# Optimization experiments

Measured on AMD Instinct MI355X. Metric: run time of the kernel, lower is better.

Reference implementation:

```python
import jax, jax.numpy as jnp
import numpy as np

BINS = 10


def _neg_pearson(p, t):
    # global standardization (torch.std default is unbiased, ddof=1)
    p = (p - p.mean()) / p.std(ddof=1)
    t = (t - t.mean()) / t.std(ddof=1)
    N = p.shape[1]
    sx = p.sum(1); sy = t.sum(1)
    sxy = (p * t).sum(1)
    sx2 = (p * p).sum(1); sy2 = (t * t).sum(1)
    pear = (N * sxy - sx * sy) / jnp.sqrt((N * sx2 - sx**2) * (N * sy2 - sy**2))
    return (1.0 - pear).mean()


def _hann(N):
    # torch.hann_window is periodic: 0.5*(1 - cos(2*pi*n/N))
    return 0.5 * (1.0 - jnp.cos(2.0 * jnp.pi * jnp.arange(N, dtype=jnp.float32) / N))


def _phase_correlation(x, t):
    # torch.stft with n_fft=seq_len, center=False, hann window -> single frame = rfft(x*hann)
    N = x.shape[1]
    w = _hann(N)
    xf = jnp.fft.rfft(x * w, axis=1)   # [B, N//2+1]
    tf = jnp.fft.rfft(t * w, axis=1)
    corr = xf * jnp.conj(tf)
    corr = corr / jnp.abs(corr)        # phase-only correlation
    cm = jnp.fft.irfft(corr, n=N, axis=1)  # [B, N]
    idx = jnp.argmax(cm, axis=1)
    return 1.0 - jnp.mean(jnp.cos(2.0 * jnp.pi * idx / N))


def _power_spectrum(x, t):
    xp = jnp.abs(jnp.fft.rfft(x, axis=1)) ** 2
    tp = jnp.abs(jnp.fft.rfft(t, axis=1)) ** 2
    return jnp.mean(jnp.abs(xp - tp)) / jnp.mean(tp)


def _mutual_information(x, y, bins=BINS):
    B, S = x.shape
    xmin = x.min(1); xmax = x.max(1)
    ymin = y.min(1); ymax = y.max(1)
    bwx = (xmax - xmin) / bins
    bwy = (ymax - ymin) / bins
    ix = jnp.clip(((x - xmin[:, None]) / bwx[:, None]).astype(jnp.int32), 0, bins - 1)
    iy = jnp.clip(((y - ymin[:, None]) / bwy[:, None]).astype(jnp.int32), 0, bins - 1)
    flat = ix * bins + iy  # [B, S]
    # vectorized 2D histogram via scatter-add (replaces the python double loop)
    hist = jax.vmap(lambda f: jnp.zeros(bins * bins, jnp.float32).at[f].add(1.0))(flat)
    hist = hist.reshape(B, bins, bins)
    hx = hist.sum(2); hy = hist.sum(1)
    denom = B * S  # NOTE: original normalizes by batch*seq (faithful reproduction)
    px = hx / denom; py = hy / denom; pxy = hist / denom
    eps = 1e-8
    mi = (pxy * jnp.log((pxy + eps) / (px[:, :, None] * py[:, None, :] + eps))).sum((1, 2))
    hxe = -(px * jnp.log(px + eps)).sum(1)
    hye = -(py * jnp.log(py + eps)).sum(1)
    nmi = mi / ((hxe + hye) / 2.0)
    return 1.0 - nmi.mean()


def setup_inputs() -> dict:
    key = jax.random.key(0)
    k1, k2 = jax.random.split(key)
    return {
        "predictions": jax.random.normal(k1, (2, 512, 16384), dtype=jnp.float32),
        "targets": jax.random.normal(k2, (512, 16384), dtype=jnp.float32),
        "i": 0,
        "epoch": 700,
    }


def reference(predictions, targets, i, epoch):
    p = predictions[i]  # [B, S]
    loss = _neg_pearson(p, targets)
    if epoch >= 400:
        loss = loss + _phase_correlation(p, targets)
        loss = loss + _power_spectrum(p, targets)
    if epoch >= 700:
        loss = loss + _mutual_information(p, targets)
    return loss
```

## Files before the change

kernel.cpp:

```cpp
#include <hip/hip_runtime.h>
#include <math.h>

#define BB 512
#define SS 16384
#define TPIF 6.28318530717958647692f

#define PD(i) ((i) + ((i) >> 4) + ((i) >> 8))
#define NPD 17472

__device__ __forceinline__ int sp(int k) {
    int s = ((k & 7) << 11) + (((k >> 3) & 7) << 8) + (((k >> 6) & 7) << 5)
          + (((k >> 9) & 7) << 2) + ((k >> 12) & 3);
    return PD(s);
}


template <int SGN, int LOG2Q>
__device__ __forceinline__ void stage_dif8(float2* sz, int t) {
    constexpr int Q = 1 << LOG2Q;
    constexpr int DQ = Q + (Q >> 4) + (Q >> 8);
    const float sg = (float)SGN;
    const float r2 = 0.70710678118654752f;
    #pragma unroll 1
    for (int c = 0; c < 2; ++c) {
        const int j = t + (c << 10);
        const int g = j >> LOG2Q;
        const int p = j & (Q - 1);
        const int i0 = PD((g << (LOG2Q + 3)) + p);
        int idx[8];
        #pragma unroll
        for (int k = 0; k < 8; ++k)
            idx[k] = (LOG2Q >= 4) ? (i0 + k * DQ) : (i0 + 4 * k + (k >> 2));
        float2 z[8];
        #pragma unroll
        for (int k = 0; k < 8; ++k) z[k] = sz[idx[k]];
        float2 a0, a1, a2, a3, b0, b1, b2, b3;
        a0 = make_float2(z[0].x + z[4].x, z[0].y + z[4].y);
        b0 = make_float2(z[0].x - z[4].x, z[0].y - z[4].y);
        a1 = make_float2(z[1].x + z[5].x, z[1].y + z[5].y);
        b1 = make_float2(z[1].x - z[5].x, z[1].y - z[5].y);
        a2 = make_float2(z[2].x + z[6].x, z[2].y + z[6].y);
        b2 = make_float2(z[2].x - z[6].x, z[2].y - z[6].y);
        a3 = make_float2(z[3].x + z[7].x, z[3].y + z[7].y);
        b3 = make_float2(z[3].x - z[7].x, z[3].y - z[7].y);
        { float x = b1.x, y = b1.y; b1 = make_float2(r2 * (x - sg * y), r2 * (y + sg * x)); }
        { float x = b2.x, y = b2.y; b2 = make_float2(-sg * y, sg * x); }
        { float x = b3.x, y = b3.y; b3 = make_float2(-r2 * (x + sg * y), r2 * (sg * x - y)); }
        float2 o[8];
        {
            float t0r = a0.x + a2.x, t0i = a0.y + a2.y;
            float t1r = a0.x - a2.x, t1i = a0.y - a2.y;
            float t2r = a1.x + a3.x, t2i = a1.y + a3.y;
            float t3r = a1.x - a3.x, t3i = a1.y - a3.y;
            o[0] = make_float2(t0r + t2r, t0i + t2i);
            o[4] = make_float2(t0r - t2r, t0i - t2i);
            o[2] = make_float2(t1r - sg * t3i, t1i + sg * t3r);
            o[6] = make_float2(t1r + sg * t3i, t1i - sg * t3r);
        }
        {
            float t0r = b0.x + b2.x, t0i = b0.y + b2.y;
            float t1r = b0.x - b2.x, t1i = b0.y - b2.y;
            float t2r = b1.x + b3.x, t2i = b1.y + b3.y;
            float t3r = b1.x - b3.x, t3i = b1.y - b3.y;
            o[1] = make_float2(t0r + t2r, t0i + t2i);
            o[5] = make_float2(t0r - t2r, t0i - t2i);
            o[3] = make_float2(t1r - sg * t3i, t1i + sg * t3r);
            o[7] = make_float2(t1r + sg * t3i, t1i - sg * t3r);
        }
        const float arev = sg * (float)p * (1.0f / (8.0f * (float)Q));
        const float cb = __builtin_amdgcn_cosf(arev);
        const float sb = __builtin_amdgcn_sinf(arev);
        sz[idx[0]] = o[0];
        float wr = cb, wi = sb;
        #pragma unroll
        for (int r = 1; r < 8; ++r) {
            sz[idx[r]] = make_float2(o[r].x * wr - o[r].y * wi,
                                     o[r].x * wi + o[r].y * wr);
            float nr = wr * cb - wi * sb, ni = wr * sb + wi * cb;
            wr = nr; wi = ni;
        }
    }
    __syncthreads();
}

template <int SGN, int LOG2Q>
__device__ __forceinline__ void stage_dit8(float2* sz, int t) {
    constexpr int Q = 1 << LOG2Q;
    constexpr int DQ = Q + (Q >> 4) + (Q >> 8);
    const float sg = (float)SGN;
    const float r2 = 0.70710678118654752f;
    #pragma unroll 1
    for (int c = 0; c < 2; ++c) {
        const int j = t + (c << 10);
        const int g = j >> LOG2Q;
        const int p = j & (Q - 1);
        const int i0 = PD((g << (LOG2Q + 3)) + p);
        int idx[8];
        #pragma unroll
        for (int k = 0; k < 8; ++k)
            idx[k] = (LOG2Q >= 4) ? (i0 + k * DQ) : (i0 + 4 * k + (k >> 2));
        const float arev = sg * (float)p * (1.0f / (8.0f * (float)Q));
        const float cb = __builtin_amdgcn_cosf(arev);
        const float sb = __builtin_amdgcn_sinf(arev);
        float2 z[8];
        z[0] = sz[idx[0]];
        float wr = cb, wi = sb;
        #pragma unroll
        for (int k = 1; k < 8; ++k) {
            float2 v = sz[idx[k]];
            z[k] = make_float2(v.x * wr - v.y * wi, v.x * wi + v.y * wr);
            float nr = wr * cb - wi * sb, ni = wr * sb + wi * cb;
            wr = nr; wi = ni;
        }
        float2 U0, U1, U2, U3, V0, V1, V2, V3;
        {
            float t0r = z[0].x + z[4].x, t0i = z[0].y + z[4].y;
            float t1r = z[0].x - z[4].x, t1i = z[0].y - z[4].y;
            float t2r = z[2].x + z[6].x, t2i = z[2].y + z[6].y;
            float t3r = z[2].x - z[6].x, t3i = z[2].y - z[6].y;
            U0 = make_float2(t0r + t2r, t0i + t2i);
            U2 = make_float2(t0r - t2r, t0i - t2i);
            U1 = make_float2(t1r - sg * t3i, t1i + sg * t3r);
            U3 = make_float2(t1r + sg * t3i, t1i - sg * t3r);
        }
        {
            float t0r = z[1].x + z[5].x, t0i = z[1].y + z[5].y;
            float t1r = z[1].x - z[5].x, t1i = z[1].y - z[5].y;
            float t2r = z[3].x + z[7].x, t2i = z[3].y + z[7].y;
            float t3r = z[3].x - z[7].x, t3i = z[3].y - z[7].y;
            V0 = make_float2(t0r + t2r, t0i + t2i);
            V2 = make_float2(t0r - t2r, t0i - t2i);
            V1 = make_float2(t1r - sg * t3i, t1i + sg * t3r);
            V3 = make_float2(t1r + sg * t3i, t1i - sg * t3r);
        }
        {
            float2 tw = V0;
            sz[idx[0]] = make_float2(U0.x + tw.x, U0.y + tw.y);
            sz[idx[4]] = make_float2(U0.x - tw.x, U0.y - tw.y);
        }
        {
            float2 tw = make_float2(r2 * (V1.x - sg * V1.y), r2 * (V1.y + sg * V1.x));
            sz[idx[1]] = make_float2(U1.x + tw.x, U1.y + tw.y);
            sz[idx[5]] = make_float2(U1.x - tw.x, U1.y - tw.y);
        }
        {
            float2 tw = make_float2(-sg * V2.y, sg * V2.x);
            sz[idx[2]] = make_float2(U2.x + tw.x, U2.y + tw.y);
            sz[idx[6]] = make_float2(U2.x - tw.x, U2.y - tw.y);
        }
        {
            float2 tw = make_float2(-r2 * (V3.x + sg * V3.y), r2 * (sg * V3.x - V3.y));
            sz[idx[3]] = make_float2(U3.x + tw.x, U3.y + tw.y);
            sz[idx[7]] = make_float2(U3.x - tw.x, U3.y - tw.y);
        }
    }
    __syncthreads();
}

template <int SGN>
__device__ __forceinline__ void stage_nt4(float2* sz, int t) {
    const float sg = (float)SGN;
    #pragma unroll 1
    for (int c = 0; c < 4; ++c) {
        const int j = t + (c << 10);
        const int i0 = 4 * j + (j >> 2) + (j >> 6);
        float2 z0 = sz[i0], z1 = sz[i0 + 1], z2 = sz[i0 + 2], z3 = sz[i0 + 3];
        float t0r = z0.x + z2.x, t0i = z0.y + z2.y;
        float t1r = z0.x - z2.x, t1i = z0.y - z2.y;
        float t2r = z1.x + z3.x, t2i = z1.y + z3.y;
        float t3r = z1.x - z3.x, t3i = z1.y - z3.y;
        sz[i0]     = make_float2(t0r + t2r, t0i + t2i);
        sz[i0 + 2] = make_float2(t0r - t2r, t0i - t2i);
        sz[i0 + 1] = make_float2(t1r - sg * t3i, t1i + sg * t3r);
        sz[i0 + 3] = make_float2(t1r + sg * t3i, t1i - sg * t3r);
    }
    __syncthreads();
}

__global__ __launch_bounds__(1024, 4) void k_main(const float* __restrict__ pred,
                                                  const float* __restrict__ targ,
                                                  const int* __restrict__ ip,
                                                  float* __restrict__ wpear,
                                                  float* __restrict__ wcos,
                                                  double* __restrict__ wnum,
                                                  double* __restrict__ wden,
                                                  float* __restrict__ wnmi) {
    __shared__ float2 sz[NPD];
    __shared__ double dpart[16 * 5];
    __shared__ float fpart[16 * 4];
    __shared__ int   subhist[400];
    __shared__ float hxm[10], hym[10];
    __shared__ float mterm[128];
    __shared__ float sbounds[4];
    __shared__ float svalw[16];
    __shared__ int   sidxw[16];

    const int row = blockIdx.x;
    const int t = threadIdx.x;
    const int w = t >> 6;
    const int lane = t & 63;

    const float* xg = pred + (size_t)ip[0] * (size_t)BB * SS + (size_t)row * SS;
    const float* yg = targ + (size_t)row * SS;

    {
        const float4* xg4 = reinterpret_cast<const float4*>(xg);
        const float4* yg4 = reinterpret_cast<const float4*>(yg);
        double sx = 0, sy = 0, sxy = 0, sxx = 0, syy = 0;
        float xmn = 3.4e38f, xmx = -3.4e38f, ymn = 3.4e38f, ymx = -3.4e38f;
        #pragma unroll
        for (int m2 = 0; m2 < 4; ++m2) {
            int idx = t + (m2 << 10);
            float4 a = xg4[idx];
            float4 b = yg4[idx];
            int n0 = idx << 2;
            sz[PD(n0 + 0)] = make_float2(a.x, b.x);
            sz[PD(n0 + 1)] = make_float2(a.y, b.y);
            sz[PD(n0 + 2)] = make_float2(a.z, b.z);
            sz[PD(n0 + 3)] = make_float2(a.w, b.w);
            float av[4] = {a.x, a.y, a.z, a.w};
            float bv[4] = {b.x, b.y, b.z, b.w};
            #pragma unroll
            for (int c = 0; c < 4; ++c) {
                float aa = av[c], bb = bv[c];
                sx += (double)aa; sy += (double)bb;
                sxy += (double)aa * (double)bb;
                sxx += (double)aa * (double)aa;
                syy += (double)bb * (double)bb;
                xmn = fminf(xmn, aa); xmx = fmaxf(xmx, aa);
                ymn = fminf(ymn, bb); ymx = fmaxf(ymx, bb);
            }
        }
        #pragma unroll
        for (int o = 32; o > 0; o >>= 1) {
            sx += __shfl_down(sx, o, 64);  sy += __shfl_down(sy, o, 64);
            sxy += __shfl_down(sxy, o, 64);
            sxx += __shfl_down(sxx, o, 64); syy += __shfl_down(syy, o, 64);
            xmn = fminf(xmn, __shfl_down(xmn, o, 64));
            xmx = fmaxf(xmx, __shfl_down(xmx, o, 64));
            ymn = fminf(ymn, __shfl_down(ymn, o, 64));
            ymx = fmaxf(ymx, __shfl_down(ymx, o, 64));
        }
        if (lane == 0) {
            dpart[w*5+0] = sx; dpart[w*5+1] = sy; dpart[w*5+2] = sxy;
            dpart[w*5+3] = sxx; dpart[w*5+4] = syy;
            fpart[w*4+0] = xmn; fpart[w*4+1] = xmx; fpart[w*4+2] = ymn; fpart[w*4+3] = ymx;
        }
    }
    if (t < 400) subhist[t] = 0;
    __syncthreads();
    if (t == 0) {
        double v0=0,v1=0,v2=0,v3=0,v4=0;
        float b0=fpart[0], b1=fpart[1], b2=fpart[2], b3=fpart[3];
        for (int q = 0; q < 16; ++q) {
            v0 += dpart[q*5]; v1 += dpart[q*5+1]; v2 += dpart[q*5+2];
            v3 += dpart[q*5+3]; v4 += dpart[q*5+4];
            b0 = fminf(b0, fpart[q*4]);   b1 = fmaxf(b1, fpart[q*4+1]);
            b2 = fminf(b2, fpart[q*4+2]); b3 = fmaxf(b3, fpart[q*4+3]);
        }
        double N = (double)SS;
        double num = N * v2 - v0 * v1;
        double den = sqrt((N * v3 - v0 * v0) * (N * v4 - v1 * v1));
        wpear[row] = (float)(1.0 - num / den);
        sbounds[0] = b0; sbounds[1] = b1; sbounds[2] = b2; sbounds[3] = b3;
    }
    __syncthreads();

    {
        const float x0 = sbounds[0], bwx = (sbounds[1] - x0) / 10.0f;
        const float y0 = sbounds[2], bwy = (sbounds[3] - y0) / 10.0f;
        int* hsub = subhist + ((t >> 6) & 3) * 100;
        #pragma unroll 2
        for (int m = 0; m < 16; ++m) {
            float2 v = sz[PD(t + (m << 10))];
            int ix = (int)((v.x - x0) / bwx); ix = min(max(ix, 0), 9);
            int iy = (int)((v.y - y0) / bwy); iy = min(max(iy, 0), 9);
            atomicAdd(&hsub[ix * 10 + iy], 1);
        }
    }
    __syncthreads();
    if (t < 100) subhist[t] = subhist[t] + subhist[100+t] + subhist[200+t] + subhist[300+t];
    __syncthreads();
    if (t < 10) {
        int s1 = 0, s2 = 0;
        for (int j = 0; j < 10; ++j) { s1 += subhist[t*10+j]; s2 += subhist[j*10+t]; }
        hxm[t] = (float)s1; hym[t] = (float)s2;
    }
    __syncthreads();
    {
        float term = 0.0f;
        if (t < 100) {
            const float denom = 8388608.0f, eps = 1e-8f;
            float pxy = (float)subhist[t] / denom;
            float px = hxm[t / 10] / denom, py = hym[t % 10] / denom;
            term = pxy * logf((pxy + eps) / (px * py + eps));
        }
        if (t < 128) mterm[t] = (t < 100) ? term : 0.0f;
    }
    __syncthreads();
    if (t == 0) {
        const float denom = 8388608.0f, eps = 1e-8f;
        float mi = 0.0f;
        for (int q = 0; q < 100; ++q) mi += mterm[q];
        float hxe = 0.0f, hye = 0.0f;
        for (int q = 0; q < 10; ++q) {
            float px = hxm[q] / denom, py = hym[q] / denom;
            hxe -= px * logf(px + eps);
            hye -= py * logf(py + eps);
        }
        wnmi[row] = mi / (0.5f * (hxe + hye));
    }
    __syncthreads();

    stage_dif8<-1, 11>(sz, t);
    stage_dif8<-1,  8>(sz, t);
    stage_dif8<-1,  5>(sz, t);
    stage_dif8<-1,  2>(sz, t);
    stage_nt4<-1>(sz, t);

    {
        double anum = 0.0, aden = 0.0;
        float crv[8], civ[8];
        #pragma unroll 1
        for (int m = 0; m < 8; ++m) {
            int k = t + (m << 10);
            int km = (SS - k) & (SS - 1);
            float2 za = sz[sp(k)];
            float2 zb = sz[sp(km)];
            float ar  = za.x, ai  = za.y;
            float cr0 = zb.x, ci0 = zb.y;
            float xr = 0.5f * (ar + cr0), xi = 0.5f * (ai - ci0);
            float yr = 0.5f * (ai + ci0), yi = 0.5f * (cr0 - ar);
            float xp = xr * xr + xi * xi;
            float tp = yr * yr + yi * yi;
            anum += (double)fabsf(xp - tp);
            aden += (double)tp;
            float2 zap = sz[sp((k + 1) & (SS - 1))];
            float2 zam = sz[sp((k - 1) & (SS - 1))];
            float2 zbp = sz[sp((km + 1) & (SS - 1))];
            float2 zbm = sz[sp((km - 1) & (SS - 1))];
            float zwr = 0.5f * ar  - 0.25f * (zap.x + zam.x);
            float zwi = 0.5f * ai  - 0.25f * (zap.y + zam.y);
            float vwr = 0.5f * cr0 - 0.25f * (zbp.x + zbm.x);
            float vwi = 0.5f * ci0 - 0.25f * (zbp.y + zbm.y);
            float xwr = 0.5f * (zwr + vwr), xwi = 0.5f * (zwi - vwi);
            float ywr = 0.5f * (zwi + vwi), ywi = 0.5f * (vwr - zwr);
            float cr = xwr * ywr + xwi * ywi;
            float ci = xwi * ywr - xwr * ywi;
            float mag = sqrtf(cr * cr + ci * ci);
            crv[m] = cr / mag; civ[m] = ci / mag;
        }
        float c8 = 0.0f;
        if (t == 0) {
            float2 z0 = sz[sp(8192)];
            float2 zp = sz[sp(8193)];
            float2 zm = sz[sp(8191)];
            float ar = z0.x, ai = z0.y;
            anum += (double)fabsf(ar * ar - ai * ai);
            aden += (double)(ai * ai);
            float zwr = 0.5f * ar - 0.25f * (zp.x + zm.x);
            float zwi = 0.5f * ai - 0.25f * (zp.y + zm.y);
            float pr = zwr * zwi;
            c8 = pr / fabsf(pr);
        }
        #pragma unroll
        for (int o = 32; o > 0; o >>= 1) {
            anum += __shfl_down(anum, o, 64);
            aden += __shfl_down(aden, o, 64);
        }
        if (lane == 0) { dpart[w*2] = anum; dpart[w*2+1] = aden; }
        __syncthreads();
        #pragma unroll
        for (int m = 0; m < 8; ++m) {
            int k = t + (m << 10);
            int km = (SS - k) & (SS - 1);
            sz[sp(k)]  = make_float2(crv[m],  civ[m]);
            sz[sp(km)] = make_float2(crv[m], -civ[m]);
        }
        if (t == 0) {
            sz[sp(8192)] = make_float2(c8, 0.0f);
            double a = 0, b = 0;
            for (int q2_ = 0; q2_ < 16; ++q2_) { a += dpart[q2_*2]; b += dpart[q2_*2+1]; }
            wnum[row] = a; wden[row] = b;
        }
    }
    __syncthreads();

    stage_nt4<1>(sz, t);
    stage_dit8<1,  2>(sz, t);
    stage_dit8<1,  5>(sz, t);
    stage_dit8<1,  8>(sz, t);
    stage_dit8<1, 11>(sz, t);

    {
        float bv = -3.4e38f; int bi = 0;
        #pragma unroll
        for (int m = 0; m < 16; ++m) {
            int n = t + (m << 10);
            float v = sz[PD(n)].x;
            if (v > bv) { bv = v; bi = n; }
        }
        #pragma unroll
        for (int o = 32; o > 0; o >>= 1) {
            float v2 = __shfl_down(bv, o, 64);
            int i2 = __shfl_down(bi, o, 64);
            if (v2 > bv || (v2 == bv && i2 < bi)) { bv = v2; bi = i2; }
        }
        if (lane == 0) { svalw[w] = bv; sidxw[w] = bi; }
    }
    __syncthreads();
    if (t == 0) {
        float bv = svalw[0]; int bi = sidxw[0];
        for (int q = 1; q < 16; ++q) {
            if (svalw[q] > bv || (svalw[q] == bv && sidxw[q] < bi)) { bv = svalw[q]; bi = sidxw[q]; }
        }
        wcos[row] = cosf(TPIF * (float)bi / 16384.0f);
    }
}

__global__ __launch_bounds__(512) void k_combine(const float* __restrict__ wpear,
                                                 const float* __restrict__ wcos,
                                                 const double* __restrict__ wnum,
                                                 const double* __restrict__ wden,
                                                 const float* __restrict__ wnmi,
                                                 const int* __restrict__ ep,
                                                 float* __restrict__ out) {
    __shared__ double dp[8 * 5];
    const int tid = threadIdx.x;
    const int w = tid >> 6, lane = tid & 63;
    double v0 = (double)wpear[tid], v1 = (double)wcos[tid];
    double v2 = wnum[tid], v3 = wden[tid], v4 = (double)wnmi[tid];
    #pragma unroll
    for (int o = 32; o > 0; o >>= 1) {
        v0 += __shfl_down(v0, o, 64); v1 += __shfl_down(v1, o, 64);
        v2 += __shfl_down(v2, o, 64); v3 += __shfl_down(v3, o, 64);
        v4 += __shfl_down(v4, o, 64);
    }
    if (lane == 0) {
        dp[w*5+0] = v0; dp[w*5+1] = v1; dp[w*5+2] = v2; dp[w*5+3] = v3; dp[w*5+4] = v4;
    }
    __syncthreads();
    if (tid == 0) {
        double s0=0,s1=0,s2=0,s3=0,s4=0;
        for (int q = 0; q < 8; ++q) {
            s0 += dp[q*5]; s1 += dp[q*5+1]; s2 += dp[q*5+2]; s3 += dp[q*5+3]; s4 += dp[q*5+4];
        }
        int epoch = ep[0];
        double loss = s0 / 512.0;
        if (epoch >= 400) {
            loss += 1.0 - s1 / 512.0;
            loss += s2 / s3;
        }
        if (epoch >= 700) {
            loss += 1.0 - s4 / 512.0;
        }
        out[0] = (float)loss;
    }
}

extern "C" void kernel_launch(void* const* d_in, const int* in_sizes, int n_in,
                              void* d_out, int out_size, void* d_ws, size_t ws_size,
                              hipStream_t stream) {
    const float* pred = (const float*)d_in[0];
    const float* targ = (const float*)d_in[1];
    const int* ip = (const int*)d_in[2];
    const int* ep = (const int*)d_in[3];
    float* out = (float*)d_out;

    double* wnum = (double*)d_ws;
    double* wden = wnum + BB;
    float* wpear = (float*)(wden + BB);
    float* wcos = wpear + BB;
    float* wnmi = wcos + BB;

    k_main<<<dim3(BB), dim3(1024), 0, stream>>>(pred, targ, ip, wpear, wcos, wnum, wden, wnmi);
    k_combine<<<dim3(1), dim3(512), 0, stream>>>(wpear, wcos, wnum, wden, wnmi, ep, out);
}
```

Measured before the change: 199.3 us.

## Compute inverse real FFT as half-length complex FFT with post-twiddle

Replaces the full 16384-point complex inverse FFT (which filled in Hermitian-mirrored bins) with the standard trick: pack the half spectrum into an 8192-point complex sequence using a twiddle pre-pass, then run a radix-8/8/8/4/4 DIF FFT on that. The real output is read as interleaved real and imaginary parts, and the argmax index is reconstructed from digit-reversed positions. This roughly halves the shared-memory traffic and butterfly work of the inverse transform, at the cost of a new pre-processing pass, a second buffer region in shared memory, and more intricate index bookkeeping.

```diff
diff --git a/kernel.cpp b/kernel.cpp
--- a/kernel.cpp
+++ b/kernel.cpp
@@ -7,6 +7,7 @@
 
 #define PD(i) ((i) + ((i) >> 4) + ((i) >> 8))
 #define NPD 17472
+#define BBASE 8200
 
 __device__ __forceinline__ int sp(int k) {
     int s = ((k & 7) << 11) + (((k >> 3) & 7) << 8) + (((k >> 6) & 7) << 5)
@@ -83,80 +84,6 @@
     __syncthreads();
 }
 
-template <int SGN, int LOG2Q>
-__device__ __forceinline__ void stage_dit8(float2* sz, int t) {
-    constexpr int Q = 1 << LOG2Q;
-    constexpr int DQ = Q + (Q >> 4) + (Q >> 8);
-    const float sg = (float)SGN;
-    const float r2 = 0.70710678118654752f;
-    #pragma unroll 1
-    for (int c = 0; c < 2; ++c) {
-        const int j = t + (c << 10);
-        const int g = j >> LOG2Q;
-        const int p = j & (Q - 1);
-        const int i0 = PD((g << (LOG2Q + 3)) + p);
-        int idx[8];
-        #pragma unroll
-        for (int k = 0; k < 8; ++k)
-            idx[k] = (LOG2Q >= 4) ? (i0 + k * DQ) : (i0 + 4 * k + (k >> 2));
-        const float arev = sg * (float)p * (1.0f / (8.0f * (float)Q));
-        const float cb = __builtin_amdgcn_cosf(arev);
-        const float sb = __builtin_amdgcn_sinf(arev);
-        float2 z[8];
-        z[0] = sz[idx[0]];
-        float wr = cb, wi = sb;
-        #pragma unroll
-        for (int k = 1; k < 8; ++k) {
-            float2 v = sz[idx[k]];
-            z[k] = make_float2(v.x * wr - v.y * wi, v.x * wi + v.y * wr);
-            float nr = wr * cb - wi * sb, ni = wr * sb + wi * cb;
-            wr = nr; wi = ni;
-        }
-        float2 U0, U1, U2, U3, V0, V1, V2, V3;
-        {
-            float t0r = z[0].x + z[4].x, t0i = z[0].y + z[4].y;
-            float t1r = z[0].x - z[4].x, t1i = z[0].y - z[4].y;
-            float t2r = z[2].x + z[6].x, t2i = z[2].y + z[6].y;
-            float t3r = z[2].x - z[6].x, t3i = z[2].y - z[6].y;
-            U0 = make_float2(t0r + t2r, t0i + t2i);
-            U2 = make_float2(t0r - t2r, t0i - t2i);
-            U1 = make_float2(t1r - sg * t3i, t1i + sg * t3r);
-            U3 = make_float2(t1r + sg * t3i, t1i - sg * t3r);
-        }
-        {
-            float t0r = z[1].x + z[5].x, t0i = z[1].y + z[5].y;
-            float t1r = z[1].x - z[5].x, t1i = z[1].y - z[5].y;
-            float t2r = z[3].x + z[7].x, t2i = z[3].y + z[7].y;
-            float t3r = z[3].x - z[7].x, t3i = z[3].y - z[7].y;
-            V0 = make_float2(t0r + t2r, t0i + t2i);
-            V2 = make_float2(t0r - t2r, t0i - t2i);
-            V1 = make_float2(t1r - sg * t3i, t1i + sg * t3r);
-            V3 = make_float2(t1r + sg * t3i, t1i - sg * t3r);
-        }
-        {
-            float2 tw = V0;
-            sz[idx[0]] = make_float2(U0.x + tw.x, U0.y + tw.y);
-            sz[idx[4]] = make_float2(U0.x - tw.x, U0.y - tw.y);
-        }
-        {
-            float2 tw = make_float2(r2 * (V1.x - sg * V1.y), r2 * (V1.y + sg * V1.x));
-            sz[idx[1]] = make_float2(U1.x + tw.x, U1.y + tw.y);
-            sz[idx[5]] = make_float2(U1.x - tw.x, U1.y - tw.y);
-        }
-        {
-            float2 tw = make_float2(-sg * V2.y, sg * V2.x);
-            sz[idx[2]] = make_float2(U2.x + tw.x, U2.y + tw.y);
-            sz[idx[6]] = make_float2(U2.x - tw.x, U2.y - tw.y);
-        }
-        {
-            float2 tw = make_float2(-r2 * (V3.x + sg * V3.y), r2 * (sg * V3.x - V3.y));
-            sz[idx[3]] = make_float2(U3.x + tw.x, U3.y + tw.y);
-            sz[idx[7]] = make_float2(U3.x - tw.x, U3.y - tw.y);
-        }
-    }
-    __syncthreads();
-}
-
 template <int SGN>
 __device__ __forceinline__ void stage_nt4(float2* sz, int t) {
     const float sg = (float)SGN;
@@ -173,6 +100,121 @@
         sz[i0 + 2] = make_float2(t0r - t2r, t0i - t2i);
         sz[i0 + 1] = make_float2(t1r - sg * t3i, t1i + sg * t3r);
         sz[i0 + 3] = make_float2(t1r + sg * t3i, t1i - sg * t3r);
+    }
+    __syncthreads();
+}
+
+template <int SGN, int LOG2Q>
+__device__ __forceinline__ void stage8k_dif8(float2* bz, int t) {
+    constexpr int Q = 1 << LOG2Q;
+    constexpr int DQ = Q + (Q >> 4) + (Q >> 8);
+    constexpr int CORR = (LOG2Q == 7) ? 1 : 0;
+    const float sg = (float)SGN;
+    const float r2 = 0.70710678118654752f;
+    const int g = t >> LOG2Q;
+    const int p = t & (Q - 1);
+    const int i0 = PD((g << (LOG2Q + 3)) + p);
+    int idx[8];
+    #pragma unroll
+    for (int k = 0; k < 8; ++k) idx[k] = i0 + k * DQ + CORR * (k >> 1);
+    float2 z[8];
+    #pragma unroll
+    for (int k = 0; k < 8; ++k) z[k] = bz[idx[k]];
+    float2 a0, a1, a2, a3, b0, b1, b2, b3;
+    a0 = make_float2(z[0].x + z[4].x, z[0].y + z[4].y);
+    b0 = make_float2(z[0].x - z[4].x, z[0].y - z[4].y);
+    a1 = make_float2(z[1].x + z[5].x, z[1].y + z[5].y);
+    b1 = make_float2(z[1].x - z[5].x, z[1].y - z[5].y);
+    a2 = make_float2(z[2].x + z[6].x, z[2].y + z[6].y);
+    b2 = make_float2(z[2].x - z[6].x, z[2].y - z[6].y);
+    a3 = make_float2(z[3].x + z[7].x, z[3].y + z[7].y);
+    b3 = make_float2(z[3].x - z[7].x, z[3].y - z[7].y);
+    { float x = b1.x, y = b1.y; b1 = make_float2(r2 * (x - sg * y), r2 * (y + sg * x)); }
+    { float x = b2.x, y = b2.y; b2 = make_float2(-sg * y, sg * x); }
+    { float x = b3.x, y = b3.y; b3 = make_float2(-r2 * (x + sg * y), r2 * (sg * x - y)); }
+    float2 o[8];
+    {
+        float t0r = a0.x + a2.x, t0i = a0.y + a2.y;
+        float t1r = a0.x - a2.x, t1i = a0.y - a2.y;
+        float t2r = a1.x + a3.x, t2i = a1.y + a3.y;
+        float t3r = a1.x - a3.x, t3i = a1.y - a3.y;
+        o[0] = make_float2(t0r + t2r, t0i + t2i);
+        o[4] = make_float2(t0r - t2r, t0i - t2i);
+        o[2] = make_float2(t1r - sg * t3i, t1i + sg * t3r);
+        o[6] = make_float2(t1r + sg * t3i, t1i - sg * t3r);
+    }
+    {
+        float t0r = b0.x + b2.x, t0i = b0.y + b2.y;
+        float t1r = b0.x - b2.x, t1i = b0.y - b2.y;
+        float t2r = b1.x + b3.x, t2i = b1.y + b3.y;
+        float t3r = b1.x - b3.x, t3i = b1.y - b3.y;
+        o[1] = make_float2(t0r + t2r, t0i + t2i);
+        o[5] = make_float2(t0r - t2r, t0i - t2i);
+        o[3] = make_float2(t1r - sg * t3i, t1i + sg * t3r);
+        o[7] = make_float2(t1r + sg * t3i, t1i - sg * t3r);
+    }
+    const float arev = sg * (float)p * (1.0f / (8.0f * (float)Q));
+    const float cb = __builtin_amdgcn_cosf(arev);
+    const float sb = __builtin_amdgcn_sinf(arev);
+    bz[idx[0]] = o[0];
+    float wr = cb, wi = sb;
+    #pragma unroll
+    for (int r = 1; r < 8; ++r) {
+        bz[idx[r]] = make_float2(o[r].x * wr - o[r].y * wi,
+                                 o[r].x * wi + o[r].y * wr);
+        float nr = wr * cb - wi * sb, ni = wr * sb + wi * cb;
+        wr = nr; wi = ni;
+    }
+    __syncthreads();
+}
+
+template <int SGN>
+__device__ __forceinline__ void stage8k_dif4(float2* bz, int t) {
+    const float sg = (float)SGN;
+    #pragma unroll 1
+    for (int c = 0; c < 2; ++c) {
+        const int j = t + (c << 10);
+        const int g = j >> 2;
+        const int p = j & 3;
+        const int i0 = PD((g << 4) + p);
+        float2 z0 = bz[i0], z1 = bz[i0 + 4], z2 = bz[i0 + 8], z3 = bz[i0 + 12];
+        float t0r = z0.x + z2.x, t0i = z0.y + z2.y;
+        float t1r = z0.x - z2.x, t1i = z0.y - z2.y;
+        float t2r = z1.x + z3.x, t2i = z1.y + z3.y;
+        float t3r = z1.x - z3.x, t3i = z1.y - z3.y;
+        float b0r = t0r + t2r, b0i = t0i + t2i;
+        float b2r = t0r - t2r, b2i = t0i - t2i;
+        float b1r = t1r - sg * t3i, b1i = t1i + sg * t3r;
+        float b3r = t1r + sg * t3i, b3i = t1i - sg * t3r;
+        const float a = sg * (float)p * (1.0f / 16.0f);
+        const float cb = __builtin_amdgcn_cosf(a);
+        const float sb = __builtin_amdgcn_sinf(a);
+        const float w2r = cb * cb - sb * sb, w2i = 2.0f * cb * sb;
+        const float w3r = cb * w2r - sb * w2i, w3i = cb * w2i + sb * w2r;
+        bz[i0]      = make_float2(b0r, b0i);
+        bz[i0 + 4]  = make_float2(b1r * cb - b1i * sb,   b1r * sb + b1i * cb);
+        bz[i0 + 8]  = make_float2(b2r * w2r - b2i * w2i, b2r * w2i + b2i * w2r);
+        bz[i0 + 12] = make_float2(b3r * w3r - b3i * w3i, b3r * w3i + b3i * w3r);
+    }
+    __syncthreads();
+}
+
+template <int SGN>
+__device__ __forceinline__ void stage8k_nt4(float2* bz, int t) {
+    const float sg = (float)SGN;
+    #pragma unroll 1
+    for (int c = 0; c < 2; ++c) {
+        const int j = t + (c << 10);
+        const int i0 = 4 * j + (j >> 2) + (j >> 6);
+        float2 z0 = bz[i0], z1 = bz[i0 + 1], z2 = bz[i0 + 2], z3 = bz[i0 + 3];
+        float t0r = z0.x + z2.x, t0i = z0.y + z2.y;
+        float t1r = z0.x - z2.x, t1i = z0.y - z2.y;
+        float t2r = z1.x + z3.x, t2i = z1.y + z3.y;
+        float t3r = z1.x - z3.x, t3i = z1.y - z3.y;
+        bz[i0]     = make_float2(t0r + t2r, t0i + t2i);
+        bz[i0 + 2] = make_float2(t0r - t2r, t0i - t2i);
+        bz[i0 + 1] = make_float2(t1r - sg * t3i, t1i + sg * t3r);
+        bz[i0 + 3] = make_float2(t1r + sg * t3i, t1i - sg * t3r);
     }
     __syncthreads();
 }
@@ -199,6 +241,7 @@
     const int t = threadIdx.x;
     const int w = t >> 6;
     const int lane = t & 63;
+    float2* bz = &sz[BBASE];
 
     const float* xg = pred + (size_t)ip[0] * (size_t)BB * SS + (size_t)row * SS;
     const float* yg = targ + (size_t)row * SS;
@@ -373,12 +416,10 @@
         #pragma unroll
         for (int m = 0; m < 8; ++m) {
             int k = t + (m << 10);
-            int km = (SS - k) & (SS - 1);
-            sz[sp(k)]  = make_float2(crv[m],  civ[m]);
-            sz[sp(km)] = make_float2(crv[m], -civ[m]);
+            sz[k] = make_float2(crv[m], civ[m]);
         }
         if (t == 0) {
-            sz[sp(8192)] = make_float2(c8, 0.0f);
+            sz[8192] = make_float2(c8, 0.0f);
             double a = 0, b = 0;
             for (int q2_ = 0; q2_ < 16; ++q2_) { a += dpart[q2_*2]; b += dpart[q2_*2+1]; }
             wnum[row] = a; wden[row] = b;
@@ -386,19 +427,46 @@
     }
     __syncthreads();
 
-    stage_nt4<1>(sz, t);
-    stage_dit8<1,  2>(sz, t);
-    stage_dit8<1,  5>(sz, t);
-    stage_dit8<1,  8>(sz, t);
-    stage_dit8<1, 11>(sz, t);
-
-    {
+    {
+        float a0 = (float)t * (1.0f / 16384.0f);
+        float wr = __builtin_amdgcn_cosf(a0);
+        float wi = __builtin_amdgcn_sinf(a0);
+        const float cs = 0.92387953251128674f;
+        const float sn = 0.38268343236508977f;
+        const int pdt = PD(t);
+        #pragma unroll 1
+        for (int c = 0; c < 8; ++c) {
+            int m = t + (c << 10);
+            float2 cm = sz[m];
+            float2 cn = sz[8192 - m];
+            float Ax = cm.x + cn.x, Ay = cm.y - cn.y;
+            float Dx = cm.x - cn.x, Dy = cm.y + cn.y;
+            float WDx = Dx * wr - Dy * wi;
+            float WDy = Dx * wi + Dy * wr;
+            bz[pdt + c * 1092] = make_float2(Ax - WDy, Ay + WDx);
+            float nr = wr * cs - wi * sn, ni = wr * sn + wi * cs;
+            wr = nr; wi = ni;
+        }
+    }
+    __syncthreads();
+
+    stage8k_dif8<1, 10>(bz, t);
+    stage8k_dif8<1,  7>(bz, t);
+    stage8k_dif8<1,  4>(bz, t);
+    stage8k_dif4<1>(bz, t);
+    stage8k_nt4<1>(bz, t);
+
+    {
+        const int K = (((t >> 7) & 7) << 3) + (((t >> 4) & 7) << 6)
+                    + (((t >> 2) & 3) << 9) + ((t & 3) << 11);
+        const int pdt = PD(t);
         float bv = -3.4e38f; int bi = 0;
         #pragma unroll
-        for (int m = 0; m < 16; ++m) {
-            int n = t + (m << 10);
-            float v = sz[PD(n)].x;
-            if (v > bv) { bv = v; bi = n; }
+        for (int c = 0; c < 8; ++c) {
+            float2 z = bz[pdt + c * 1092];
+            int n2 = (K + c) << 1;
+            if (z.x > bv) { bv = z.x; bi = n2; }
+            if (z.y > bv) { bv = z.y; bi = n2 + 1; }
         }
         #pragma unroll
         for (int o = 32; o > 0; o >>= 1) {
```

New measurement: 190.3 us. -4.5%, faster.
